# Optimization experiments

Hardware: AMD Instinct MI355X
Metric: run time of the kernel (lower is better)

## Reference

```python
import jax, jax.numpy as jnp
import numpy as np

B, D, H, W, K = 32, 128, 128, 128, 32

def setup_inputs() -> dict:
    key = jax.random.key(0)
    k1, k2, k3 = jax.random.split(key, 3)
    X = jax.random.normal(k1, (B, D, H, W), dtype=jnp.float32)
    std1 = 1.0 / np.sqrt(K * D)
    codewords = jax.random.uniform(k2, (K, D), dtype=jnp.float32, minval=-std1, maxval=std1)
    scale = jax.random.uniform(k3, (K,), dtype=jnp.float32, minval=-1.0, maxval=0.0)
    return {"X": X, "codewords": codewords, "scale": scale}

def reference(X, codewords, scale):
    # X: [B, D, H, W] -> [B, N, D]
    b, d = X.shape[0], X.shape[1]
    x = X.reshape(b, d, -1).transpose(0, 2, 1)  # [B, N, D]
    x2 = jnp.sum(x * x, axis=-1, keepdims=True)            # [B, N, 1]
    c2 = jnp.sum(codewords * codewords, axis=-1)           # [K]
    xc = jnp.einsum('bnd,kd->bnk', x, codewords)           # [B, N, K]
    sl = scale * (x2 - 2.0 * xc + c2)                      # [B, N, K]
    A = jax.nn.softmax(sl, axis=2)                         # assignment weights
    # E[b,k,d] = sum_n A[b,n,k] * (x[b,n,d] - c[k,d])
    E = jnp.einsum('bnk,bnd->bkd', A, x) - jnp.sum(A, axis=1)[..., None] * codewords
    return E
```

## Files before the change

kernel.cpp:

```cpp
#include <hip/hip_runtime.h>
#include <hip/hip_bf16.h>

#define B_   32
#define D_   128
#define N_   16384
#define K_   32
#define NS   256
#define AST_STRIDE 264

#define WS_WBF  0
#define WS_SC   2048
#define WS_C2S  2080
#define WS_EP   2112

typedef __attribute__((ext_vector_type(8))) short bf16x8;
typedef __attribute__((ext_vector_type(4))) float f32x4;

static __device__ inline unsigned int pk2(float lo, float hi) {
    __hip_bfloat162 h = __float22bfloat162_rn(make_float2(lo, hi));
    unsigned int r;
    __builtin_memcpy(&r, &h, 4);
    return r;
}

static __device__ inline bf16x8 pack8(const float* v) {
    union { unsigned int u[4]; bf16x8 f; } r;
    r.u[0] = pk2(v[0], v[1]);
    r.u[1] = pk2(v[2], v[3]);
    r.u[2] = pk2(v[4], v[5]);
    r.u[3] = pk2(v[6], v[7]);
    return r.f;
}

__global__ void prep_kernel(const float* __restrict__ cw,
                            const float* __restrict__ scale,
                            float* __restrict__ ws) {
    const int k = blockIdx.x;
    const int l = threadIdx.x;
    const float sc = scale[k] * 1.44269504088896f;
    unsigned short* Wbf = (unsigned short*)(ws + WS_WBF);
    float s = 0.f;
#pragma unroll
    for (int i = 0; i < 2; ++i) {
        const int d = l + i * 64;
        const float v = cw[k * D_ + d];
        s += v * v;
        const float w = -2.f * sc * v;
        unsigned int u = __float_as_uint(w);
        u += 0x7fffu + ((u >> 16) & 1u);
        Wbf[k * D_ + d] = (unsigned short)(u >> 16);
    }
#pragma unroll
    for (int o = 32; o > 0; o >>= 1) s += __shfl_down(s, o, 64);
    if (l == 0) {
        ws[WS_SC  + k] = sc;
        ws[WS_C2S + k] = sc * s;
    }
}

template<int NCHUNKT>
__global__ __launch_bounds__(256, 4) void main_kernel(
        const float* __restrict__ X,
        const float* __restrict__ ws_ro,
        float* __restrict__ AsumP,
        float* __restrict__ Ep)
{
    constexpr int CSZT  = N_ / NCHUNKT;
    constexpr int NSUBT = CSZT / NS;

    __shared__ __align__(16) unsigned short AsT[K_ * AST_STRIDE];

    const int t    = threadIdx.x;
    const int lane = t & 63;
    const int w    = t >> 6;
    const int mc   = lane & 15;
    const int q    = lane >> 4;

    const int blk   = blockIdx.x;
    const int b     = blk / NCHUNKT;
    const int chunk = blk % NCHUNKT;
    const int n0    = chunk * CSZT;

    const float* Xb = X + (size_t)b * ((size_t)D_ * N_);

    const unsigned short* Wbf = (const unsigned short*)(ws_ro + WS_WBF);
    bf16x8 wf[2][4];
#pragma unroll
    for (int kb = 0; kb < 2; ++kb)
#pragma unroll
        for (int kd = 0; kd < 4; ++kd)
            wf[kb][kd] = *(const bf16x8*)&Wbf[(kb * 16 + mc) * D_ + kd * 32 + q * 8];

    float scr[2][4], c2r[2][4];
#pragma unroll
    for (int kb = 0; kb < 2; ++kb)
#pragma unroll
        for (int r = 0; r < 4; ++r) {
            scr[kb][r] = ws_ro[WS_SC  + kb * 16 + q * 4 + r];
            c2r[kb][r] = ws_ro[WS_C2S + kb * 16 + q * 4 + r];
        }

    bf16x8 ones;
#pragma unroll
    for (int i = 0; i < 8; ++i) ones[i] = (short)0x3F80;

    f32x4 accE[2][2] = {{{0.f,0.f,0.f,0.f},{0.f,0.f,0.f,0.f}},
                        {{0.f,0.f,0.f,0.f},{0.f,0.f,0.f,0.f}}};
    f32x4 accO[2]    = {{0.f,0.f,0.f,0.f},{0.f,0.f,0.f,0.f}};

    for (int s = 0; s < NSUBT; ++s) {
        const int ns = n0 + s * NS;

#pragma unroll 1
        for (int cb = 0; cb < 4; ++cb) {
            const int ntl = (w * 4 + cb) * 16;
            const float* xp = Xb + ns + ntl + mc;

            f32x4 S0 = {0.f,0.f,0.f,0.f};
            f32x4 S1 = {0.f,0.f,0.f,0.f};
            float x2 = 0.f;
#pragma unroll
            for (int kd = 0; kd < 4; ++kd) {
                float xv[8];
#pragma unroll
                for (int j = 0; j < 8; ++j)
                    xv[j] = xp[(size_t)(kd * 32 + q * 8 + j) * N_];
#pragma unroll
                for (int j = 0; j < 8; ++j) x2 = fmaf(xv[j], xv[j], x2);
                const bf16x8 xb = pack8(xv);
                S0 = __builtin_amdgcn_mfma_f32_16x16x32_bf16(wf[0][kd], xb, S0, 0, 0, 0);
                S1 = __builtin_amdgcn_mfma_f32_16x16x32_bf16(wf[1][kd], xb, S1, 0, 0, 0);
            }
            x2 += __shfl_xor(x2, 16, 64);
            x2 += __shfl_xor(x2, 32, 64);

            float sl[8];
#pragma unroll
            for (int r = 0; r < 4; ++r) {
                sl[r]     = fmaf(scr[0][r], x2, S0[r] + c2r[0][r]);
                sl[4 + r] = fmaf(scr[1][r], x2, S1[r] + c2r[1][r]);
            }
            float m = sl[0];
#pragma unroll
            for (int i = 1; i < 8; ++i) m = fmaxf(m, sl[i]);
            m = fmaxf(m, __shfl_xor(m, 16, 64));
            m = fmaxf(m, __shfl_xor(m, 32, 64));
            float ssum = 0.f;
#pragma unroll
            for (int i = 0; i < 8; ++i) { sl[i] = exp2f(sl[i] - m); ssum += sl[i]; }
            ssum += __shfl_xor(ssum, 16, 64);
            ssum += __shfl_xor(ssum, 32, 64);
            const float inv = 1.f / ssum;

            const int col = ntl + mc;
#pragma unroll
            for (int r = 0; r < 4; ++r) {
                const unsigned int u = pk2(sl[r] * inv, sl[4 + r] * inv);
                AsT[(q * 4 + r) * AST_STRIDE + col]        = (unsigned short)u;
                AsT[(16 + q * 4 + r) * AST_STRIDE + col]   = (unsigned short)(u >> 16);
            }
        }
        __syncthreads();

        const int dq = w;
#pragma unroll 2
        for (int ks = 0; ks < NS / 32; ++ks) {
            const int nl = ks * 32 + q * 8;
            const bf16x8 a0 = *(const bf16x8*)&AsT[mc * AST_STRIDE + nl];
            const bf16x8 a1 = *(const bf16x8*)&AsT[(16 + mc) * AST_STRIDE + nl];

            const float* bp = Xb + (size_t)(dq * 32 + mc) * N_ + ns + nl;
            float xr[8];
            *(float4*)&xr[0] = *(const float4*)bp;
            *(float4*)&xr[4] = *(const float4*)(bp + 4);
            const bf16x8 xb0 = pack8(xr);
            const float* bp2 = bp + (size_t)16 * N_;
            *(float4*)&xr[0] = *(const float4*)bp2;
            *(float4*)&xr[4] = *(const float4*)(bp2 + 4);
            const bf16x8 xb1 = pack8(xr);

            accE[0][0] = __builtin_amdgcn_mfma_f32_16x16x32_bf16(a0, xb0, accE[0][0], 0, 0, 0);
            accE[0][1] = __builtin_amdgcn_mfma_f32_16x16x32_bf16(a0, xb1, accE[0][1], 0, 0, 0);
            accE[1][0] = __builtin_amdgcn_mfma_f32_16x16x32_bf16(a1, xb0, accE[1][0], 0, 0, 0);
            accE[1][1] = __builtin_amdgcn_mfma_f32_16x16x32_bf16(a1, xb1, accE[1][1], 0, 0, 0);
            if (w == 0) {
                accO[0] = __builtin_amdgcn_mfma_f32_16x16x32_bf16(a0, ones, accO[0], 0, 0, 0);
                accO[1] = __builtin_amdgcn_mfma_f32_16x16x32_bf16(a1, ones, accO[1], 0, 0, 0);
            }
        }
        __syncthreads();
    }

    float* EpB = Ep + (size_t)blk * (K_ * D_);
#pragma unroll
    for (int kh = 0; kh < 2; ++kh)
#pragma unroll
        for (int ds = 0; ds < 2; ++ds)
#pragma unroll
            for (int r = 0; r < 4; ++r) {
                const int k = kh * 16 + q * 4 + r;
                const int d = w * 32 + ds * 16 + mc;
                EpB[k * D_ + d] = accE[kh][ds][r];
            }
    if (w == 0 && mc == 0) {
#pragma unroll
        for (int kh = 0; kh < 2; ++kh)
#pragma unroll
            for (int r = 0; r < 4; ++r)
                AsumP[blk * K_ + kh * 16 + q * 4 + r] = accO[kh][r];
    }
}

template<int NCHUNKT>
__global__ void finalize_kernel(const float* __restrict__ cw,
                                const float* __restrict__ AsumP,
                                const float* __restrict__ Ep,
                                float* __restrict__ out)
{
    const int idx = blockIdx.x * 256 + threadIdx.x;
    const int d = idx & 127;
    const int k = (idx >> 7) & 31;
    const int b = idx >> 12;
    float s = 0.f, asum = 0.f;
#pragma unroll
    for (int c = 0; c < NCHUNKT; ++c) {
        const int blk = b * NCHUNKT + c;
        s    += Ep[(size_t)blk * (K_ * D_) + k * D_ + d];
        asum += AsumP[blk * K_ + k];
    }
    out[idx] = s - asum * cw[k * D_ + d];
}

extern "C" void kernel_launch(void* const* d_in, const int* in_sizes, int n_in,
                              void* d_out, int out_size, void* d_ws, size_t ws_size,
                              hipStream_t stream) {
    const float* X     = (const float*)d_in[0];
    const float* cw    = (const float*)d_in[1];
    const float* scale = (const float*)d_in[2];
    float* out = (float*)d_out;
    float* ws  = (float*)d_ws;

    prep_kernel<<<K_, 64, 0, stream>>>(cw, scale, ws);

    const size_t need32 = (size_t)(WS_EP + 1024 * (K_ * D_) + 1024 * K_) * 4;
    if (ws_size >= need32) {
        float* Ep    = ws + WS_EP;
        float* AsumP = Ep + (size_t)1024 * (K_ * D_);
        main_kernel<32><<<B_ * 32, 256, 0, stream>>>(X, ws, AsumP, Ep);
        finalize_kernel<32><<<(B_ * K_ * D_) / 256, 256, 0, stream>>>(cw, AsumP, Ep, out);
    } else {
        float* Ep    = ws + WS_EP;
        float* AsumP = Ep + (size_t)512 * (K_ * D_);
        main_kernel<16><<<B_ * 16, 256, 0, stream>>>(X, ws, AsumP, Ep);
        finalize_kernel<16><<<(B_ * K_ * D_) / 256, 256, 0, stream>>>(cw, AsumP, Ep, out);
    }
}
```

Measured before the change: 422.6 us.

## Load X once per subtile into LDS as bf16 and reuse for both GEMMs

Instead of reading X from global memory twice (strided column loads for the distance GEMM, row loads for the aggregation GEMM), each subtile is loaded once with coalesced vector loads and converted to bf16. The result is kept in registers for the aggregation MFMAs and written transposed into a new LDS buffer for the distance stage. The subtile size is halved to fit LDS, launch bounds drop to 3 waves per SIMD, and ||x||^2 is now computed from bf16-rounded values. The trailing barrier is removed, which relies on the next iteration's barrier to order AsT reuse; this is a possible race risk.

```diff
diff --git a/kernel.cpp b/kernel.cpp
--- a/kernel.cpp
+++ b/kernel.cpp
@@ -5,8 +5,9 @@
 #define D_   128
 #define N_   16384
 #define K_   32
-#define NS   256
-#define AST_STRIDE 264
+#define NS   128
+#define XS_STRIDE 136
+#define AST_STRIDE 136
 
 #define WS_WBF  0
 #define WS_SC   2048
@@ -23,12 +24,12 @@
     return r;
 }
 
-static __device__ inline bf16x8 pack8(const float* v) {
+static __device__ inline bf16x8 pack8v(f32x4 a, f32x4 b) {
     union { unsigned int u[4]; bf16x8 f; } r;
-    r.u[0] = pk2(v[0], v[1]);
-    r.u[1] = pk2(v[2], v[3]);
-    r.u[2] = pk2(v[4], v[5]);
-    r.u[3] = pk2(v[6], v[7]);
+    r.u[0] = pk2(a[0], a[1]);
+    r.u[1] = pk2(a[2], a[3]);
+    r.u[2] = pk2(b[0], b[1]);
+    r.u[3] = pk2(b[2], b[3]);
     return r.f;
 }
 
@@ -59,7 +60,7 @@
 }
 
 template<int NCHUNKT>
-__global__ __launch_bounds__(256, 4) void main_kernel(
+__global__ __launch_bounds__(256, 3) void main_kernel(
         const float* __restrict__ X,
         const float* __restrict__ ws_ro,
         float* __restrict__ AsumP,
@@ -68,6 +69,7 @@
     constexpr int CSZT  = N_ / NCHUNKT;
     constexpr int NSUBT = CSZT / NS;
 
+    __shared__ __align__(16) unsigned short Xs[NS * XS_STRIDE];
     __shared__ __align__(16) unsigned short AsT[K_ * AST_STRIDE];
 
     const int t    = threadIdx.x;
@@ -108,29 +110,66 @@
                         {{0.f,0.f,0.f,0.f},{0.f,0.f,0.f,0.f}}};
     f32x4 accO[2]    = {{0.f,0.f,0.f,0.f},{0.f,0.f,0.f,0.f}};
 
+    const float* xr0 = Xb + (size_t)(w * 32 + mc) * N_ + n0 + q * 8;
+    const int dA = w * 32 + mc;
+
     for (int s = 0; s < NSUBT; ++s) {
-        const int ns = n0 + s * NS;
-
-#pragma unroll 1
-        for (int cb = 0; cb < 4; ++cb) {
-            const int ntl = (w * 4 + cb) * 16;
-            const float* xp = Xb + ns + ntl + mc;
+        const float* xp = xr0 + s * NS;
+        bf16x8 xf0[4], xf1[4];
+#pragma unroll
+        for (int ks = 0; ks < 4; ++ks) {
+            const f32x4 a0 = *(const f32x4*)(xp + ks * 32);
+            const f32x4 b0 = *(const f32x4*)(xp + ks * 32 + 4);
+            const f32x4 a1 = *(const f32x4*)(xp + ks * 32 + (size_t)16 * N_);
+            const f32x4 b1 = *(const f32x4*)(xp + ks * 32 + (size_t)16 * N_ + 4);
+            xf0[ks] = pack8v(a0, b0);
+            xf1[ks] = pack8v(a1, b1);
+        }
+#pragma unroll
+        for (int ks = 0; ks < 4; ++ks) {
+            union { bf16x8 f; unsigned int u[4]; } ua, ub;
+            ua.f = xf0[ks];
+            ub.f = xf1[ks];
+            const int base = (ks * 32 + q * 8) * XS_STRIDE + dA;
+#pragma unroll
+            for (int j2 = 0; j2 < 4; ++j2) {
+                Xs[base + (2*j2)   * XS_STRIDE]      = (unsigned short)(ua.u[j2]);
+                Xs[base + (2*j2+1) * XS_STRIDE]      = (unsigned short)(ua.u[j2] >> 16);
+                Xs[base + (2*j2)   * XS_STRIDE + 16] = (unsigned short)(ub.u[j2]);
+                Xs[base + (2*j2+1) * XS_STRIDE + 16] = (unsigned short)(ub.u[j2] >> 16);
+            }
+        }
+        __syncthreads();
+
+#pragma unroll
+        for (int cb = 0; cb < NS / 64; ++cb) {
+            const int ntl  = (w * (NS / 64) + cb) * 16;
+            const int rowb = (ntl + mc) * XS_STRIDE;
+
+            union fr { bf16x8 f; unsigned int u[4]; } xb[4];
+#pragma unroll
+            for (int kd = 0; kd < 4; ++kd)
+                xb[kd].f = *(const bf16x8*)&Xs[rowb + kd * 32 + q * 8];
+
+            float x2 = 0.f;
+#pragma unroll
+            for (int kd = 0; kd < 4; ++kd)
+#pragma unroll
+                for (int wd = 0; wd < 4; ++wd) {
+                    const float lo = __uint_as_float(xb[kd].u[wd] << 16);
+                    const float hi = __uint_as_float(xb[kd].u[wd] & 0xffff0000u);
+                    x2 = fmaf(lo, lo, x2);
+                    x2 = fmaf(hi, hi, x2);
+                }
 
             f32x4 S0 = {0.f,0.f,0.f,0.f};
             f32x4 S1 = {0.f,0.f,0.f,0.f};
-            float x2 = 0.f;
 #pragma unroll
             for (int kd = 0; kd < 4; ++kd) {
-                float xv[8];
-#pragma unroll
-                for (int j = 0; j < 8; ++j)
-                    xv[j] = xp[(size_t)(kd * 32 + q * 8 + j) * N_];
-#pragma unroll
-                for (int j = 0; j < 8; ++j) x2 = fmaf(xv[j], xv[j], x2);
-                const bf16x8 xb = pack8(xv);
-                S0 = __builtin_amdgcn_mfma_f32_16x16x32_bf16(wf[0][kd], xb, S0, 0, 0, 0);
-                S1 = __builtin_amdgcn_mfma_f32_16x16x32_bf16(wf[1][kd], xb, S1, 0, 0, 0);
-            }
+                S0 = __builtin_amdgcn_mfma_f32_16x16x32_bf16(wf[0][kd], xb[kd].f, S0, 0, 0, 0);
+                S1 = __builtin_amdgcn_mfma_f32_16x16x32_bf16(wf[1][kd], xb[kd].f, S1, 0, 0, 0);
+            }
+
             x2 += __shfl_xor(x2, 16, 64);
             x2 += __shfl_xor(x2, 32, 64);
 
@@ -156,39 +195,26 @@
 #pragma unroll
             for (int r = 0; r < 4; ++r) {
                 const unsigned int u = pk2(sl[r] * inv, sl[4 + r] * inv);
-                AsT[(q * 4 + r) * AST_STRIDE + col]        = (unsigned short)u;
-                AsT[(16 + q * 4 + r) * AST_STRIDE + col]   = (unsigned short)(u >> 16);
+                AsT[(q * 4 + r) * AST_STRIDE + col]      = (unsigned short)u;
+                AsT[(16 + q * 4 + r) * AST_STRIDE + col] = (unsigned short)(u >> 16);
             }
         }
         __syncthreads();
 
-        const int dq = w;
-#pragma unroll 2
+#pragma unroll
         for (int ks = 0; ks < NS / 32; ++ks) {
             const int nl = ks * 32 + q * 8;
             const bf16x8 a0 = *(const bf16x8*)&AsT[mc * AST_STRIDE + nl];
             const bf16x8 a1 = *(const bf16x8*)&AsT[(16 + mc) * AST_STRIDE + nl];
-
-            const float* bp = Xb + (size_t)(dq * 32 + mc) * N_ + ns + nl;
-            float xr[8];
-            *(float4*)&xr[0] = *(const float4*)bp;
-            *(float4*)&xr[4] = *(const float4*)(bp + 4);
-            const bf16x8 xb0 = pack8(xr);
-            const float* bp2 = bp + (size_t)16 * N_;
-            *(float4*)&xr[0] = *(const float4*)bp2;
-            *(float4*)&xr[4] = *(const float4*)(bp2 + 4);
-            const bf16x8 xb1 = pack8(xr);
-
-            accE[0][0] = __builtin_amdgcn_mfma_f32_16x16x32_bf16(a0, xb0, accE[0][0], 0, 0, 0);
-            accE[0][1] = __builtin_amdgcn_mfma_f32_16x16x32_bf16(a0, xb1, accE[0][1], 0, 0, 0);
-            accE[1][0] = __builtin_amdgcn_mfma_f32_16x16x32_bf16(a1, xb0, accE[1][0], 0, 0, 0);
-            accE[1][1] = __builtin_amdgcn_mfma_f32_16x16x32_bf16(a1, xb1, accE[1][1], 0, 0, 0);
+            accE[0][0] = __builtin_amdgcn_mfma_f32_16x16x32_bf16(a0, xf0[ks], accE[0][0], 0, 0, 0);
+            accE[0][1] = __builtin_amdgcn_mfma_f32_16x16x32_bf16(a0, xf1[ks], accE[0][1], 0, 0, 0);
+            accE[1][0] = __builtin_amdgcn_mfma_f32_16x16x32_bf16(a1, xf0[ks], accE[1][0], 0, 0, 0);
+            accE[1][1] = __builtin_amdgcn_mfma_f32_16x16x32_bf16(a1, xf1[ks], accE[1][1], 0, 0, 0);
             if (w == 0) {
                 accO[0] = __builtin_amdgcn_mfma_f32_16x16x32_bf16(a0, ones, accO[0], 0, 0, 0);
                 accO[1] = __builtin_amdgcn_mfma_f32_16x16x32_bf16(a1, ones, accO[1], 0, 0, 0);
             }
         }
-        __syncthreads();
     }
 
     float* EpB = Ep + (size_t)blk * (K_ * D_);
```

New measurement: 396.7 us. -6.1%, faster.
